# Kernel tuning notes

Measured on AMD Instinct MI355X. Metric: run time of the kernel, lower is better.

Reference implementation:

```python
import jax, jax.numpy as jnp
import numpy as np

VOCAB = 200000
E = 128   # embedding_size
H = 128   # lstm_hidden_size
OH = 1024 # output_hidden_size
B = 256   # pair batch
L = 256   # per-sentence length


def setup_inputs() -> dict:
    key = jax.random.key(0)
    ks = jax.random.split(key, 8)
    return {
        "s1": jax.random.randint(ks[0], (B, L), 0, VOCAB, dtype=jnp.int32),
        "s2": jax.random.randint(ks[1], (B, L), 0, VOCAB, dtype=jnp.int32),
        "emb_W": jax.random.normal(ks[2], (VOCAB, E), jnp.float32) * 0.1,
        "W_fwd": jax.random.normal(ks[3], (E + H, 4 * H), jnp.float32) * 0.1,
        "b_fwd": jnp.zeros((4 * H,), jnp.float32),
        "W_bwd": jax.random.normal(ks[4], (E + H, 4 * H), jnp.float32) * 0.1,
        "b_bwd": jnp.zeros((4 * H,), jnp.float32),
        "W_mid": jax.random.normal(ks[5], (4 * H, OH), jnp.float32) * 0.1,
        "b_mid": jnp.zeros((OH,), jnp.float32),
        "W_out": jax.random.normal(ks[6], (OH, 1), jnp.float32) * 0.1,
        "b_out": jnp.zeros((1,), jnp.float32),
    }


def _reverse_sequence(x, lens):
    # x: [N, T, ...]; reverse first lens[n] steps of each row (tf.reverse_sequence)
    T = x.shape[1]
    t = jnp.arange(T)[None, :]                      # [1, T]
    idx = jnp.where(t < lens[:, None], lens[:, None] - 1 - t, t)  # [N, T]
    return jnp.take_along_axis(x, idx[..., None], axis=1)


def _lstm(x, lens, W, b):
    # x: [N, T, E]; BasicLSTMCell with forget_bias=1.0, zeros past lens (dynamic_rnn)
    N, T, _ = x.shape
    x_tm = jnp.swapaxes(x, 0, 1)                    # [T, N, E]
    ts = jnp.arange(T)
    h0 = jnp.zeros((N, H), x.dtype)
    c0 = jnp.zeros((N, H), x.dtype)

    def step(carry, inp):
        h, c = carry
        xt, t = inp
        z = jnp.concatenate([xt, h], axis=-1) @ W + b
        i, j, f, o = jnp.split(z, 4, axis=-1)
        nc = c * jax.nn.sigmoid(f + 1.0) + jax.nn.sigmoid(i) * jnp.tanh(j)
        nh = jnp.tanh(nc) * jax.nn.sigmoid(o)
        m = (t < lens)[:, None]
        return (jnp.where(m, nh, h), jnp.where(m, nc, c)), jnp.where(m, nh, 0.0)

    _, ys = jax.lax.scan(step, (h0, c0), (x_tm, ts))
    return jnp.swapaxes(ys, 0, 1)                   # [N, T, H]


def reference(s1, s2, emb_W, W_fwd, b_fwd, W_bwd, b_bwd, W_mid, b_mid, W_out, b_out):
    # input_concat: [B, 2L] -> [2B, L]
    inp = jnp.concatenate([s1, s2], axis=1).reshape(-1, L)       # [2B, L]
    lens = jnp.sum(inp != 0, axis=1)                              # count_nonzero
    emb = emb_W[inp]                                              # [2B, L, E]

    out_f = _lstm(emb, lens, W_fwd, b_fwd)                        # [2B, L, H]
    # backward dir: reverse_sequence -> lstm -> reverse_sequence (bidirectional_dynamic_rnn)
    out_b = _reverse_sequence(_lstm(_reverse_sequence(emb, lens), lens, W_bwd, b_bwd), lens)
    # original graph applies an extra full tf.reverse on the backward output
    lstm_out = jnp.concatenate([out_f, jnp.flip(out_b, axis=1)], axis=2)  # [2B, L, 2H]

    seq_vec = jnp.mean(lstm_out, axis=1)                          # [2B, 2H]
    feats = seq_vec.reshape(-1, 4 * H)                            # [B, 4H]
    hid = jax.nn.relu(feats @ W_mid + b_mid)
    logits = hid @ W_out + b_out                                  # [B, 1]
    return jax.nn.sigmoid(logits).reshape(-1)                     # [B]
```

## Files before the change

kernel.cpp:

```cpp
#include <hip/hip_runtime.h>
#include <stdint.h>
#include <stddef.h>


typedef short short8 __attribute__((ext_vector_type(8)));
typedef float f32x4  __attribute__((ext_vector_type(4)));

#define LSEQ 256
#define NCOL 512
#define RS   288
#define ABUF (4 * RS)

#define MFMA(A, B, C) __builtin_amdgcn_mfma_f32_16x16x32_bf16((A), (B), (C), 0, 0, 0)

__device__ __forceinline__ unsigned short f2bf(float f) {
    unsigned u = __builtin_bit_cast(unsigned, f);
    u += 0x7fffu + ((u >> 16) & 1u);
    return (unsigned short)(u >> 16);
}
__device__ __forceinline__ float sigm(float x) {
    float t = __builtin_amdgcn_exp2f(-1.4426950408889634f * x);
    return __builtin_amdgcn_rcpf(1.0f + t);
}

__global__ __launch_bounds__(1024, 4)
void bilstm_kernel(const int* __restrict__ s1, const int* __restrict__ s2,
                   const float* __restrict__ embW,
                   const float* __restrict__ Wf, const float* __restrict__ bf_,
                   const float* __restrict__ Wb, const float* __restrict__ bb_,
                   float* __restrict__ seqvec ) {
    const int tid  = threadIdx.x;
    const int lane = tid & 63;
    const int wave = tid >> 6;
    const int dir   = blockIdx.x & 1;
    const int sbase = (blockIdx.x >> 1) * 4;

    const float* __restrict__ W    = dir ? Wb  : Wf;
    const float* __restrict__ bias = dir ? bb_ : bf_;

    __shared__ char xb[2 * ABUF];
    __shared__ char hb[2 * ABUF];
    __shared__ int  tokRaw[4][LSEQ];
    __shared__ int  tokR[4][LSEQ];
    __shared__ int  lenS[4];

    const int c = lane & 15;
    const int g = lane >> 4;
    const int unit = wave * 8 + (c & 7);

    if (tid < ABUF / 16) *(short8*)(hb + ABUF + tid * 16) = (short8)0;

    int mylen = 0;
    if (wave < 4) {
        const int n = sbase + wave;
        const int* src = (n & 1) ? (s2 + (size_t)(n >> 1) * LSEQ)
                                 : (s1 + (size_t)(n >> 1) * LSEQ);
        const int4 tk = *(const int4*)(src + lane * 4);
        *(int4*)&tokRaw[wave][lane * 4] = tk;
        int cnt = (tk.x != 0) + (tk.y != 0) + (tk.z != 0) + (tk.w != 0);
        #pragma unroll
        for (int s = 1; s < 64; s <<= 1) cnt += __shfl_xor(cnt, s, 64);
        mylen = cnt;
        if (lane == 0) lenS[wave] = cnt;
        #pragma unroll
        for (int r = 0; r < 4; ++r) {
            const int t   = r * 64 + lane;
            const int idx = dir ? ((t < mylen) ? (mylen - 1 - t) : t) : t;
            tokR[wave][t] = tokRaw[wave][idx];
        }
        #pragma unroll
        for (int s = 0; s < 2; ++s) {
            const int tk2 = tokR[wave][s];
            const float2 xv = *(const float2*)(embW + (size_t)tk2 * 128 + lane * 2);
            *(unsigned*)(xb + s * ABUF + wave * RS + lane * 4) =
                (unsigned)f2bf(xv.x) | ((unsigned)f2bf(xv.y) << 16);
        }
    }

    const int colnt0 = (c < 8) ? unit : (256 + unit);
    const int colnt1 = (c < 8) ? (128 + unit) : (384 + unit);

    short8 wfrag[8][2];
    #pragma unroll
    for (int kk = 0; kk < 8; ++kk) {
        #pragma unroll
        for (int nt = 0; nt < 2; ++nt) {
            const int col = nt ? colnt1 : colnt0;
            short8 v;
            #pragma unroll
            for (int j = 0; j < 8; ++j)
                v[j] = (short)f2bf(W[(size_t)(kk * 32 + g * 8 + j) * NCOL + col]);
            f32x4 tmp = __builtin_bit_cast(f32x4, v);
            asm volatile("" : "+v"(tmp));
            wfrag[kk][nt] = __builtin_bit_cast(short8, tmp);
        }
    }
    const float b0s = bias[colnt0] + ((c >= 8) ? 1.0f : 0.0f);
    const float b1s = bias[colnt1];
    const f32x4 biasv0 = {b0s, b0s, b0s, b0s};
    const f32x4 biasv1 = {b1s, b1s, b1s, b1s};

    const float km1 = (c < 8) ? -2.8853900817779268f : -1.4426950408889634f;
    const float a1c = (c < 8) ? 2.0f : 1.0f;
    const float b1c = (c < 8) ? -1.0f : 0.0f;
    const float KM0 = -1.4426950408889634f;
    const float KM2 = -2.8853900817779268f;

    const int ard = (c & 3) * RS + g * 16;
    const int hwr = g * RS + unit * 2;
    const int xst = wave * RS + lane * 4;

    __syncthreads();

    f32x4 zxa, zxb;
    {
        const short8 x0 = *(const short8*)(xb + ard);
        const short8 x1 = *(const short8*)(xb + ard + 64);
        const short8 x2 = *(const short8*)(xb + ard + 128);
        const short8 x3 = *(const short8*)(xb + ard + 192);
        zxa = MFMA(x0, wfrag[0][0], biasv0);  zxb = MFMA(x0, wfrag[0][1], biasv1);
        zxa = MFMA(x1, wfrag[1][0], zxa);     zxb = MFMA(x1, wfrag[1][1], zxb);
        zxa = MFMA(x2, wfrag[2][0], zxa);     zxb = MFMA(x2, wfrag[2][1], zxb);
        zxa = MFMA(x3, wfrag[3][0], zxa);     zxb = MFMA(x3, wfrag[3][1], zxb);
    }
    __syncthreads();

    const int lenv = lenS[g];
    float cs = 0.f, sm = 0.f, hs = 0.f;

    auto STEP = [&](int t, const char* hR, char* hW, const char* xR, char* xW) {
        float2 xv;
        if (wave < 4) {
            const int tp = (t + 2 < LSEQ) ? t + 2 : LSEQ - 1;
            const int tk = tokR[wave][tp];
            xv = *(const float2*)(embW + (size_t)tk * 128 + lane * 2);
        }

        const short8 h0 = *(const short8*)(hR + ard);
        const short8 h1 = *(const short8*)(hR + ard + 64);
        const short8 h2 = *(const short8*)(hR + ard + 128);
        const short8 h3 = *(const short8*)(hR + ard + 192);
        f32x4 a = MFMA(h0, wfrag[4][0], zxa);
        f32x4 b = MFMA(h0, wfrag[4][1], zxb);
        a = MFMA(h1, wfrag[5][0], a);  b = MFMA(h1, wfrag[5][1], b);
        a = MFMA(h2, wfrag[6][0], a);  b = MFMA(h2, wfrag[6][1], b);
        a = MFMA(h3, wfrag[7][0], a);  b = MFMA(h3, wfrag[7][1], b);

        const float zc0 = (g < 2) ? ((g == 0) ? a[0] : a[1])
                                  : ((g == 2) ? a[2] : a[3]);
        const float zc1 = (g < 2) ? ((g == 0) ? b[0] : b[1])
                                  : ((g == 2) ? b[2] : b[3]);

        const short8 x0 = *(const short8*)(xR + ard);
        const short8 x1 = *(const short8*)(xR + ard + 64);
        const short8 x2 = *(const short8*)(xR + ard + 128);
        const short8 x3 = *(const short8*)(xR + ard + 192);

        const float e0  = __builtin_amdgcn_exp2f(KM0 * zc0);
        const float g0v = __builtin_amdgcn_rcpf(1.0f + e0);
        const float e1  = __builtin_amdgcn_exp2f(km1 * zc1);
        const float g1v = a1c * __builtin_amdgcn_rcpf(1.0f + e1) + b1c;
        const float pr  = g0v * g1v;
        const float prx = __shfl_xor(pr, 8, 64);

        zxa = MFMA(x0, wfrag[0][0], biasv0);  zxb = MFMA(x0, wfrag[0][1], biasv1);
        zxa = MFMA(x1, wfrag[1][0], zxa);     zxb = MFMA(x1, wfrag[1][1], zxb);
        zxa = MFMA(x2, wfrag[2][0], zxa);     zxb = MFMA(x2, wfrag[2][1], zxb);
        zxa = MFMA(x3, wfrag[3][0], zxa);     zxb = MFMA(x3, wfrag[3][1], zxb);

        const bool  v  = (t < lenv);
        const float nc = cs * g0v + prx;
        const float er = __builtin_amdgcn_exp2f(KM2 * nc);
        const float th = 2.0f * __builtin_amdgcn_rcpf(1.0f + er) - 1.0f;
        const float nh = th * g1v;
        cs = v ? nc : cs;
        sm += v ? nh : 0.0f;
        hs = v ? nh : hs;

        if (c >= 8) *(unsigned short*)(hW + hwr) = f2bf(hs);
        if (wave < 4)
            *(unsigned*)(xW + xst) =
                (unsigned)f2bf(xv.x) | ((unsigned)f2bf(xv.y) << 16);
        __syncthreads();
    };

    for (int tt = 0; tt < LSEQ; tt += 2) {
        STEP(tt,     hb + ABUF, hb,        xb + ABUF, xb);
        STEP(tt + 1, hb,        hb + ABUF, xb,        xb + ABUF);
    }

    if (c >= 8)
        seqvec[(size_t)(sbase + g) * 256 + dir * 128 + unit] = sm * (1.0f / 256.0f);
}

__global__ __launch_bounds__(256)
void mlp_part(const float* __restrict__ feats,
              const float* __restrict__ Wm, const float* __restrict__ bm,
              const float* __restrict__ Wo,
              float* __restrict__ partials ) {
    const int tid  = threadIdx.x;
    const int lane = tid & 63;
    const int ct   = blockIdx.x & 3;
    const int p0   = (blockIdx.x >> 2) * 4;
    const int pair = p0 + (tid >> 6);
    const int col4 = ct * 256 + lane * 4;
    __shared__ float fe[4][512];

    {
        float* fef = &fe[0][0];
        const float* src = feats + (size_t)p0 * 512;
        *(float4*)&fef[tid * 8]     = *(const float4*)(src + tid * 8);
        *(float4*)&fef[tid * 8 + 4] = *(const float4*)(src + tid * 8 + 4);
    }
    __syncthreads();

    f32x4 ac0 = {0,0,0,0}, ac1 = {0,0,0,0}, ac2 = {0,0,0,0}, ac3 = {0,0,0,0};
    for (int k = 0; k < 512; k += 4) {
        const f32x4 w0 = *(const f32x4*)(Wm + (size_t)(k + 0) * 1024 + col4);
        const f32x4 w1 = *(const f32x4*)(Wm + (size_t)(k + 1) * 1024 + col4);
        const f32x4 w2 = *(const f32x4*)(Wm + (size_t)(k + 2) * 1024 + col4);
        const f32x4 w3 = *(const f32x4*)(Wm + (size_t)(k + 3) * 1024 + col4);
        ac0 += w0 * fe[pair - p0][k + 0];
        ac1 += w1 * fe[pair - p0][k + 1];
        ac2 += w2 * fe[pair - p0][k + 2];
        ac3 += w3 * fe[pair - p0][k + 3];
    }
    const f32x4 acc = (ac0 + ac1) + (ac2 + ac3);
    const f32x4 bm4 = *(const f32x4*)(bm + col4);
    const f32x4 wo4 = *(const f32x4*)(Wo + col4);
    float part = 0.f;
    #pragma unroll
    for (int q = 0; q < 4; ++q)
        part += fmaxf(acc[q] + bm4[q], 0.f) * wo4[q];

    #pragma unroll
    for (int s = 1; s < 64; s <<= 1) part += __shfl_xor(part, s, 64);
    if (lane == 0) partials[ct * 256 + pair] = part;
}

__global__ __launch_bounds__(256)
void mlp_fin(const float* __restrict__ partials,
             const float* __restrict__ bo, float* __restrict__ out) {
    const int p = threadIdx.x;
    out[p] = sigm(partials[p] + partials[256 + p] + partials[512 + p] +
                  partials[768 + p] + bo[0]);
}

extern "C" void kernel_launch(void* const* d_in, const int* in_sizes, int n_in,
                              void* d_out, int out_size, void* d_ws, size_t ws_size,
                              hipStream_t stream) {
    const int*   s1   = (const int*)d_in[0];
    const int*   s2   = (const int*)d_in[1];
    const float* embW = (const float*)d_in[2];
    const float* Wf   = (const float*)d_in[3];
    const float* bf_  = (const float*)d_in[4];
    const float* Wb   = (const float*)d_in[5];
    const float* bb_  = (const float*)d_in[6];
    const float* Wm   = (const float*)d_in[7];
    const float* bm   = (const float*)d_in[8];
    const float* Wo   = (const float*)d_in[9];
    const float* bo   = (const float*)d_in[10];

    float* seqvec   = (float*)d_ws;
    float* partials = seqvec + 512 * 256;

    bilstm_kernel<<<256, 1024, 0, stream>>>(s1, s2, embW, Wf, bf_, Wb, bb_, seqvec);
    mlp_part<<<256, 256, 0, stream>>>(seqvec, Wm, bm, Wo, partials);
    mlp_fin<<<1, 256, 0, stream>>>(partials, bo, (float*)d_out);
}
```

Baseline: 383.7 us.

## Halve LSTM block to 8 waves, each wave computing all four gates per unit

Each wave now owns 16 hidden units and computes all four gate tiles (i,j,f,o) itself, instead of splitting gates across lane halves and exchanging products with a cross-lane shuffle. The block shrinks from 16 to 8 waves, so fewer waves take part in each per-step barrier and no shuffle is needed. In exchange each wave issues twice as many MFMAs per step, holds twice the weight fragments in registers, and every lane evaluates three sigmoids plus a tanh.

```diff
diff --git a/kernel.cpp b/kernel.cpp
--- a/kernel.cpp
+++ b/kernel.cpp
@@ -23,7 +23,7 @@
     return __builtin_amdgcn_rcpf(1.0f + t);
 }
 
-__global__ __launch_bounds__(1024, 4)
+__global__ __launch_bounds__(512, 2)
 void bilstm_kernel(const int* __restrict__ s1, const int* __restrict__ s2,
                    const float* __restrict__ embW,
                    const float* __restrict__ Wf, const float* __restrict__ bf_,
@@ -46,7 +46,7 @@
 
     const int c = lane & 15;
     const int g = lane >> 4;
-    const int unit = wave * 8 + (c & 7);
+    const int u = wave * 16 + c;
 
     if (tid < ABUF / 16) *(short8*)(hb + ABUF + tid * 16) = (short8)0;
 
@@ -77,15 +77,12 @@
         }
     }
 
-    const int colnt0 = (c < 8) ? unit : (256 + unit);
-    const int colnt1 = (c < 8) ? (128 + unit) : (384 + unit);
-
-    short8 wfrag[8][2];
+    short8 wfrag[8][4];
     #pragma unroll
     for (int kk = 0; kk < 8; ++kk) {
         #pragma unroll
-        for (int nt = 0; nt < 2; ++nt) {
-            const int col = nt ? colnt1 : colnt0;
+        for (int nt = 0; nt < 4; ++nt) {
+            const int col = nt * 128 + u;
             short8 v;
             #pragma unroll
             for (int j = 0; j < 8; ++j)
@@ -95,33 +92,38 @@
             wfrag[kk][nt] = __builtin_bit_cast(short8, tmp);
         }
     }
-    const float b0s = bias[colnt0] + ((c >= 8) ? 1.0f : 0.0f);
-    const float b1s = bias[colnt1];
-    const f32x4 biasv0 = {b0s, b0s, b0s, b0s};
-    const f32x4 biasv1 = {b1s, b1s, b1s, b1s};
-
-    const float km1 = (c < 8) ? -2.8853900817779268f : -1.4426950408889634f;
-    const float a1c = (c < 8) ? 2.0f : 1.0f;
-    const float b1c = (c < 8) ? -1.0f : 0.0f;
-    const float KM0 = -1.4426950408889634f;
-    const float KM2 = -2.8853900817779268f;
+    const float bi = bias[u];
+    const float bj = bias[128 + u];
+    const float bf = bias[256 + u] + 1.0f;
+    const float bo = bias[384 + u];
+    const f32x4 Bi = {bi, bi, bi, bi};
+    const f32x4 Bj = {bj, bj, bj, bj};
+    const f32x4 Bf = {bf, bf, bf, bf};
+    const f32x4 Bo = {bo, bo, bo, bo};
+
+    const float KS = -1.4426950408889634f;
+    const float KT = -2.8853900817779268f;
 
     const int ard = (c & 3) * RS + g * 16;
-    const int hwr = g * RS + unit * 2;
+    const int hwr = g * RS + u * 2;
     const int xst = wave * RS + lane * 4;
 
     __syncthreads();
 
-    f32x4 zxa, zxb;
+    f32x4 zi, zj, zf, zo;
     {
         const short8 x0 = *(const short8*)(xb + ard);
         const short8 x1 = *(const short8*)(xb + ard + 64);
         const short8 x2 = *(const short8*)(xb + ard + 128);
         const short8 x3 = *(const short8*)(xb + ard + 192);
-        zxa = MFMA(x0, wfrag[0][0], biasv0);  zxb = MFMA(x0, wfrag[0][1], biasv1);
-        zxa = MFMA(x1, wfrag[1][0], zxa);     zxb = MFMA(x1, wfrag[1][1], zxb);
-        zxa = MFMA(x2, wfrag[2][0], zxa);     zxb = MFMA(x2, wfrag[2][1], zxb);
-        zxa = MFMA(x3, wfrag[3][0], zxa);     zxb = MFMA(x3, wfrag[3][1], zxb);
+        zi = MFMA(x0, wfrag[0][0], Bi); zj = MFMA(x0, wfrag[0][1], Bj);
+        zf = MFMA(x0, wfrag[0][2], Bf); zo = MFMA(x0, wfrag[0][3], Bo);
+        zi = MFMA(x1, wfrag[1][0], zi); zj = MFMA(x1, wfrag[1][1], zj);
+        zf = MFMA(x1, wfrag[1][2], zf); zo = MFMA(x1, wfrag[1][3], zo);
+        zi = MFMA(x2, wfrag[2][0], zi); zj = MFMA(x2, wfrag[2][1], zj);
+        zf = MFMA(x2, wfrag[2][2], zf); zo = MFMA(x2, wfrag[2][3], zo);
+        zi = MFMA(x3, wfrag[3][0], zi); zj = MFMA(x3, wfrag[3][1], zj);
+        zf = MFMA(x3, wfrag[3][2], zf); zo = MFMA(x3, wfrag[3][3], zo);
     }
     __syncthreads();
 
@@ -140,44 +142,47 @@
         const short8 h1 = *(const short8*)(hR + ard + 64);
         const short8 h2 = *(const short8*)(hR + ard + 128);
         const short8 h3 = *(const short8*)(hR + ard + 192);
-        f32x4 a = MFMA(h0, wfrag[4][0], zxa);
-        f32x4 b = MFMA(h0, wfrag[4][1], zxb);
-        a = MFMA(h1, wfrag[5][0], a);  b = MFMA(h1, wfrag[5][1], b);
-        a = MFMA(h2, wfrag[6][0], a);  b = MFMA(h2, wfrag[6][1], b);
-        a = MFMA(h3, wfrag[7][0], a);  b = MFMA(h3, wfrag[7][1], b);
-
-        const float zc0 = (g < 2) ? ((g == 0) ? a[0] : a[1])
-                                  : ((g == 2) ? a[2] : a[3]);
-        const float zc1 = (g < 2) ? ((g == 0) ? b[0] : b[1])
-                                  : ((g == 2) ? b[2] : b[3]);
+        f32x4 ai = MFMA(h0, wfrag[4][0], zi), aj = MFMA(h0, wfrag[4][1], zj);
+        f32x4 af = MFMA(h0, wfrag[4][2], zf), ao = MFMA(h0, wfrag[4][3], zo);
+        ai = MFMA(h1, wfrag[5][0], ai); aj = MFMA(h1, wfrag[5][1], aj);
+        af = MFMA(h1, wfrag[5][2], af); ao = MFMA(h1, wfrag[5][3], ao);
+        ai = MFMA(h2, wfrag[6][0], ai); aj = MFMA(h2, wfrag[6][1], aj);
+        af = MFMA(h2, wfrag[6][2], af); ao = MFMA(h2, wfrag[6][3], ao);
+        ai = MFMA(h3, wfrag[7][0], ai); aj = MFMA(h3, wfrag[7][1], aj);
+        af = MFMA(h3, wfrag[7][2], af); ao = MFMA(h3, wfrag[7][3], ao);
+
+        const float zci = (g < 2) ? ((g == 0) ? ai[0] : ai[1]) : ((g == 2) ? ai[2] : ai[3]);
+        const float zcj = (g < 2) ? ((g == 0) ? aj[0] : aj[1]) : ((g == 2) ? aj[2] : aj[3]);
+        const float zcf = (g < 2) ? ((g == 0) ? af[0] : af[1]) : ((g == 2) ? af[2] : af[3]);
+        const float zco = (g < 2) ? ((g == 0) ? ao[0] : ao[1]) : ((g == 2) ? ao[2] : ao[3]);
 
         const short8 x0 = *(const short8*)(xR + ard);
         const short8 x1 = *(const short8*)(xR + ard + 64);
         const short8 x2 = *(const short8*)(xR + ard + 128);
         const short8 x3 = *(const short8*)(xR + ard + 192);
-
-        const float e0  = __builtin_amdgcn_exp2f(KM0 * zc0);
-        const float g0v = __builtin_amdgcn_rcpf(1.0f + e0);
-        const float e1  = __builtin_amdgcn_exp2f(km1 * zc1);
-        const float g1v = a1c * __builtin_amdgcn_rcpf(1.0f + e1) + b1c;
-        const float pr  = g0v * g1v;
-        const float prx = __shfl_xor(pr, 8, 64);
-
-        zxa = MFMA(x0, wfrag[0][0], biasv0);  zxb = MFMA(x0, wfrag[0][1], biasv1);
-        zxa = MFMA(x1, wfrag[1][0], zxa);     zxb = MFMA(x1, wfrag[1][1], zxb);
-        zxa = MFMA(x2, wfrag[2][0], zxa);     zxb = MFMA(x2, wfrag[2][1], zxb);
-        zxa = MFMA(x3, wfrag[3][0], zxa);     zxb = MFMA(x3, wfrag[3][1], zxb);
+        zi = MFMA(x0, wfrag[0][0], Bi); zj = MFMA(x0, wfrag[0][1], Bj);
+        zf = MFMA(x0, wfrag[0][2], Bf); zo = MFMA(x0, wfrag[0][3], Bo);
+        zi = MFMA(x1, wfrag[1][0], zi); zj = MFMA(x1, wfrag[1][1], zj);
+        zf = MFMA(x1, wfrag[1][2], zf); zo = MFMA(x1, wfrag[1][3], zo);
+        zi = MFMA(x2, wfrag[2][0], zi); zj = MFMA(x2, wfrag[2][1], zj);
+        zf = MFMA(x2, wfrag[2][2], zf); zo = MFMA(x2, wfrag[2][3], zo);
+        zi = MFMA(x3, wfrag[3][0], zi); zj = MFMA(x3, wfrag[3][1], zj);
+        zf = MFMA(x3, wfrag[3][2], zf); zo = MFMA(x3, wfrag[3][3], zo);
+
+        const float I = __builtin_amdgcn_rcpf(1.0f + __builtin_amdgcn_exp2f(KS * zci));
+        const float F = __builtin_amdgcn_rcpf(1.0f + __builtin_amdgcn_exp2f(KS * zcf));
+        const float O = __builtin_amdgcn_rcpf(1.0f + __builtin_amdgcn_exp2f(KS * zco));
+        const float J = 2.0f * __builtin_amdgcn_rcpf(1.0f + __builtin_amdgcn_exp2f(KT * zcj)) - 1.0f;
 
         const bool  v  = (t < lenv);
-        const float nc = cs * g0v + prx;
-        const float er = __builtin_amdgcn_exp2f(KM2 * nc);
-        const float th = 2.0f * __builtin_amdgcn_rcpf(1.0f + er) - 1.0f;
-        const float nh = th * g1v;
+        const float nc = cs * F + I * J;
+        const float th = 2.0f * __builtin_amdgcn_rcpf(1.0f + __builtin_amdgcn_exp2f(KT * nc)) - 1.0f;
+        const float nh = th * O;
         cs = v ? nc : cs;
         sm += v ? nh : 0.0f;
         hs = v ? nh : hs;
 
-        if (c >= 8) *(unsigned short*)(hW + hwr) = f2bf(hs);
+        *(unsigned short*)(hW + hwr) = f2bf(hs);
         if (wave < 4)
             *(unsigned*)(xW + xst) =
                 (unsigned)f2bf(xv.x) | ((unsigned)f2bf(xv.y) << 16);
@@ -189,8 +194,7 @@
         STEP(tt + 1, hb,        hb + ABUF, xb,        xb + ABUF);
     }
 
-    if (c >= 8)
-        seqvec[(size_t)(sbase + g) * 256 + dir * 128 + unit] = sm * (1.0f / 256.0f);
+    seqvec[(size_t)(sbase + g) * 256 + dir * 128 + u] = sm * (1.0f / 256.0f);
 }
 
 __global__ __launch_bounds__(256)
@@ -264,7 +268,7 @@
     float* seqvec   = (float*)d_ws;
     float* partials = seqvec + 512 * 256;
 
-    bilstm_kernel<<<256, 1024, 0, stream>>>(s1, s2, embW, Wf, bf_, Wb, bb_, seqvec);
+    bilstm_kernel<<<256, 512, 0, stream>>>(s1, s2, embW, Wf, bf_, Wb, bb_, seqvec);
     mlp_part<<<256, 256, 0, stream>>>(seqvec, Wm, bm, Wo, partials);
     mlp_fin<<<1, 256, 0, stream>>>(partials, bo, (float*)d_out);
 }
```

Result: no change. 382.3 us (-0.3%).
